# Performance work log

Measured on AMD Instinct MI355X. Metric: run time of the kernel, lower is better.

## Reference

```python
import jax, jax.numpy as jnp
import numpy as np

B, S, IN, E, L = 8, 1024, 768, 256, 12

def setup_inputs() -> dict:
    key = jax.random.key(0)
    k1, k2, k3, k4 = jax.random.split(key, 4)
    input_tensor = jax.random.normal(k1, (B, S, IN), dtype=jnp.float32)
    fc_w = jax.random.normal(k2, (E, IN), dtype=jnp.float32) * (1.0 / np.sqrt(IN))
    fc_b = jax.random.normal(k3, (E,), dtype=jnp.float32) * 0.02
    bi_w = jax.random.normal(k4, (E * L, E), dtype=jnp.float32) * (1.0 / np.sqrt(E))
    bias = jnp.zeros((E,), dtype=jnp.float32)
    return {"input_tensor": input_tensor, "fc_w": fc_w, "fc_b": fc_b, "bi_w": bi_w, "bias": bias}

def reference(input_tensor, fc_w, fc_b, bi_w, bias):
    # fc: [B,S,IN] -> [B,S,E]
    t = jnp.einsum('bsi,ei->bse', input_tensor, fc_w) + fc_b
    # bi_linear: [B,S,E] -> [B,S,L,E], plus bias over E
    bl = jnp.einsum('bse,fe->bsf', t, bi_w).reshape(B, S, L, E) + bias
    # bilinear score: out[b,i,l,j] = sum_e bl[b,i,l,e] * t[b,j,e]
    # (avoids materializing the O(B*S*S*E) expanded value tensor)
    return jnp.einsum('bile,bje->bilj', bl, t)
```

## Files before the change

kernel.cpp:

```cpp
#include <hip/hip_runtime.h>
#include <hip/hip_bf16.h>

typedef __bf16 bf16_t;
typedef __bf16 bf16x8 __attribute__((ext_vector_type(8)));
typedef __bf16 bf16x4 __attribute__((ext_vector_type(4)));
typedef float f32x4 __attribute__((ext_vector_type(4)));

#define AS1 __attribute__((address_space(1)))
#define AS3 __attribute__((address_space(3)))

__global__ __launch_bounds__(256)
void cvt_all(const float* __restrict__ in, bf16_t* __restrict__ o_in,
             const float* __restrict__ fw, bf16_t* __restrict__ o_fw,
             const float* __restrict__ bw, bf16_t* __restrict__ o_bw) {
    int i = blockIdx.x * 256 + threadIdx.x;
    const float* s;
    bf16_t* d;
    int k;
    if (i < 786432)      { s = in; d = o_in; k = i; }
    else if (i < 811008) { s = fw; d = o_fw; k = i - 786432; }
    else if (i < 909312) { s = bw; d = o_bw; k = i - 811008; }
    else return;
    float4 a = ((const float4*)s)[k * 2];
    float4 b = ((const float4*)s)[k * 2 + 1];
    bf16x8 v;
    v[0] = (bf16_t)a.x; v[1] = (bf16_t)a.y; v[2] = (bf16_t)a.z; v[3] = (bf16_t)a.w;
    v[4] = (bf16_t)b.x; v[5] = (bf16_t)b.y; v[6] = (bf16_t)b.z; v[7] = (bf16_t)b.w;
    ((bf16x8*)d)[k] = v;
}

template <int BM, int BN, int EPI>
__global__ __launch_bounds__(256)
void gemm_bt(const bf16_t* __restrict__ A, const bf16_t* __restrict__ Bm,
             void* __restrict__ Cv, const float* __restrict__ bias,
             int M, int N, int K) {
    constexpr int MR = BM / 32;
    constexpr int NR = BN / 32;
    typedef float fvec __attribute__((ext_vector_type(NR)));
    typedef bf16_t bvec __attribute__((ext_vector_type(NR)));

    __shared__ bf16_t As[BM * 64];
    __shared__ bf16_t Bs[BN * 64];

    const int tid  = threadIdx.x;
    const int lane = tid & 63;
    const int wave = tid >> 6;
    const int mblk = blockIdx.x, nblk = blockIdx.y;

    const bf16_t* Ab = A + (long)mblk * BM * K;
    const bf16_t* Bb = Bm + (long)nblk * BN * K;

    f32x4 acc[MR][NR] = {};

    const int wrow = (wave >> 1) * (BM / 2);
    const int wcol = (wave & 1) * (BN / 2);
    const int lrow = lane & 15;
    const int kgrp = lane >> 4;

    for (int k0 = 0; k0 < K; k0 += 64) {
#pragma unroll
        for (int it = 0; it < MR; ++it) {
            const int chunk = it * 256 + tid;
            const int row = chunk >> 3, c8 = chunk & 7;
            __builtin_amdgcn_global_load_lds(
                (const AS1 void*)(Ab + (long)row * K + k0 + c8 * 8),
                (AS3 void*)(As + chunk * 8), 16, 0, 0);
        }
#pragma unroll
        for (int it = 0; it < NR; ++it) {
            const int chunk = it * 256 + tid;
            const int row = chunk >> 3, c8 = chunk & 7;
            __builtin_amdgcn_global_load_lds(
                (const AS1 void*)(Bb + (long)row * K + k0 + c8 * 8),
                (AS3 void*)(Bs + chunk * 8), 16, 0, 0);
        }
        __syncthreads();

#pragma unroll
        for (int kk = 0; kk < 64; kk += 32) {
            const int koff = kk + kgrp * 8;
            bf16x8 af[MR], bfr[NR];
#pragma unroll
            for (int m = 0; m < MR; ++m)
                af[m] = *(const bf16x8*)(As + (wrow + m * 16 + lrow) * 64 + koff);
#pragma unroll
            for (int n = 0; n < NR; ++n)
                bfr[n] = *(const bf16x8*)(Bs + (wcol + lrow * NR + n) * 64 + koff);
#pragma unroll
            for (int m = 0; m < MR; ++m)
#pragma unroll
                for (int n = 0; n < NR; ++n)
                    acc[m][n] = __builtin_amdgcn_mfma_f32_16x16x32_bf16(af[m], bfr[n], acc[m][n], 0, 0, 0);
        }
        __syncthreads();
    }

    const long rbase = (long)mblk * BM + wrow + kgrp * 4;
    const long cb0   = (long)nblk * BN + wcol + lrow * NR;
    bf16_t* C = (bf16_t*)Cv;
    const float* bp = bias + cb0;
    fvec bv = *(const fvec*)bp;
#pragma unroll
    for (int m = 0; m < MR; ++m)
#pragma unroll
        for (int j = 0; j < 4; ++j) {
            bvec v;
#pragma unroll
            for (int n = 0; n < NR; ++n) v[n] = (bf16_t)(acc[m][n][j] + bv[n]);
            *(bvec*)(C + (rbase + m * 16 + j) * N + cb0) = v;
        }
}

template <int EPI, int XCD, int NMB, int NNB>
__global__ __launch_bounds__(512, 2)
void gemm8p(const bf16_t* __restrict__ A, const bf16_t* __restrict__ Bm,
            void* __restrict__ Cv, const float* __restrict__ bias,
            int N, long sA, long sB, long sC) {
    constexpr int K = 256;
    extern __shared__ bf16_t lds[];

    const int tid  = threadIdx.x;
    const int lane = tid & 63;
    const int wave = tid >> 6;
    const int wm = wave >> 2, wn = wave & 3;
    const int lrow = lane & 15, kgrp = lane >> 4;

    int mblk, nblk, bz;
    {
        int L = blockIdx.x;
        if (XCD) { bz = L & 7; int w = L >> 3; nblk = w % NNB; mblk = w / NNB; }
        else     { bz = 0;     mblk = L % NMB; nblk = L / NMB; }
    }

    const bf16_t* Ab = A + (long)bz * sA + (long)mblk * 256 * K;
    const bf16_t* Bb = Bm + (long)bz * sB + (long)nblk * 256 * K;

    const int c0 = tid, c1 = 512 + tid;
    const int r0 = c0 >> 3, r1 = c1 >> 3;
    const int ca0 = (c0 & 7) ^ (r0 & 7),        ca1 = (c1 & 7) ^ (r1 & 7);
    const int cb0 = (c0 & 7) ^ ((r0 >> 2) & 7), cb1 = (c1 & 7) ^ ((r1 >> 2) & 7);

    auto stageA = [&](int t, int h) {
        const bf16_t* s0 = Ab + (long)(h * 128 + r0) * K + t * 64 + ca0 * 8;
        const bf16_t* s1 = Ab + (long)(h * 128 + r1) * K + t * 64 + ca1 * 8;
        bf16_t* d = lds + ((t & 1) * 2 + h) * 8192;
        __builtin_amdgcn_global_load_lds((const AS1 void*)s0, (AS3 void*)(d + c0 * 8), 16, 0, 0);
        __builtin_amdgcn_global_load_lds((const AS1 void*)s1, (AS3 void*)(d + c1 * 8), 16, 0, 0);
    };
    auto stageB = [&](int t, int h) {
        const bf16_t* s0 = Bb + (long)(h * 128 + r0) * K + t * 64 + cb0 * 8;
        const bf16_t* s1 = Bb + (long)(h * 128 + r1) * K + t * 64 + cb1 * 8;
        bf16_t* d = lds + 32768 + ((t & 1) * 2 + h) * 8192;
        __builtin_amdgcn_global_load_lds((const AS1 void*)s0, (AS3 void*)(d + c0 * 8), 16, 0, 0);
        __builtin_amdgcn_global_load_lds((const AS1 void*)s1, (AS3 void*)(d + c1 * 8), 16, 0, 0);
    };
    auto ldA = [&](int t, int mf, int kk) -> bf16x8 {
        const int row = mf * 16 + lrow;
        const int col = (kk * 32 + kgrp * 8) ^ ((row & 7) << 3);
        return *(const bf16x8*)(lds + ((t & 1) * 2 + wm) * 8192 + row * 64 + col);
    };
    auto ldB = [&](int t, int g, int kk) -> bf16x8 {
        const int row = (wn & 1) * 64 + lrow * 4 + g;
        const int col = (kk * 32 + kgrp * 8) ^ (((row >> 2) & 7) << 3);
        return *(const bf16x8*)(lds + 32768 + ((t & 1) * 2 + (wn >> 1)) * 8192 + row * 64 + col);
    };

    f32x4 acc[8][4] = {};
    bf16x8 bfr[4][2];

    stageA(0, 0); stageA(0, 1); stageB(0, 0); stageB(0, 1); stageB(1, 0); stageB(1, 1);
    asm volatile("s_waitcnt vmcnt(4)" ::: "memory");
    __builtin_amdgcn_s_barrier();

#pragma unroll
    for (int i = 0; i < 2; ++i) {
#pragma unroll
        for (int p = 0; p < 8; ++p) {
            const int q = p & 3;
            const int t = 2 * i + (p >> 2);
            bf16x8 af[2][2];
            if (q == 0) {
#pragma unroll
                for (int g = 0; g < 4; ++g) { bfr[g][0] = ldB(t, g, 0); bfr[g][1] = ldB(t, g, 1); }
            }
#pragma unroll
            for (int mm = 0; mm < 2; ++mm) { af[mm][0] = ldA(t, 2 * q + mm, 0); af[mm][1] = ldA(t, 2 * q + mm, 1); }

            if (p == 0) stageA(2 * i + 1, 0);
            else if (p == 1) stageA(2 * i + 1, 1);
            else if (p == 2) { if (2 * i + 2 < 4) stageB(2 * i + 2, 0); }
            else if (p == 3) { if (2 * i + 2 < 4) stageB(2 * i + 2, 1); }
            else if (p == 4) { if (2 * i + 2 < 4) stageA(2 * i + 2, 0); }
            else if (p == 5) { if (2 * i + 2 < 4) stageA(2 * i + 2, 1); }
            else if (p == 6) { if (2 * i + 3 < 4) stageB(2 * i + 3, 0); }
            else             { if (2 * i + 3 < 4) stageB(2 * i + 3, 1); }

            __builtin_amdgcn_s_barrier();
            asm volatile("s_waitcnt lgkmcnt(0)" ::: "memory");
            __builtin_amdgcn_s_setprio(1);
#pragma unroll
            for (int mm = 0; mm < 2; ++mm)
#pragma unroll
                for (int g = 0; g < 4; ++g)
#pragma unroll
                    for (int kk = 0; kk < 2; ++kk)
                        acc[2 * q + mm][g] = __builtin_amdgcn_mfma_f32_16x16x32_bf16(
                            af[mm][kk], bfr[g][kk], acc[2 * q + mm][g], 0, 0, 0);
            __builtin_amdgcn_s_setprio(0);

            if (p == 3) {
                if (2 * i + 2 < 4) asm volatile("s_waitcnt vmcnt(4)" ::: "memory");
                else               asm volatile("s_waitcnt vmcnt(0)" ::: "memory");
            } else if (p == 7) {
                if (2 * i + 2 < 4) asm volatile("s_waitcnt vmcnt(4)" ::: "memory");
            }
            __builtin_amdgcn_s_barrier();
        }
    }

    const long rb = (long)mblk * 256 + wm * 128 + kgrp * 4;
    const long cb = (long)nblk * 256 + wn * 64 + lrow * 4;
    if constexpr (EPI == 0) {
        float* C = (float*)Cv + (long)bz * sC;
#pragma unroll
        for (int m = 0; m < 8; ++m)
#pragma unroll
            for (int j = 0; j < 4; ++j) {
                f32x4 v = { acc[m][0][j], acc[m][1][j], acc[m][2][j], acc[m][3][j] };
                __builtin_nontemporal_store(v, (f32x4*)(C + (rb + m * 16 + j) * N + cb));
            }
    } else {
        bf16_t* C = (bf16_t*)Cv;
        f32x4 bv = *(const f32x4*)(bias + (int)(cb & 255));
#pragma unroll
        for (int m = 0; m < 8; ++m)
#pragma unroll
            for (int j = 0; j < 4; ++j) {
                bf16x4 v;
#pragma unroll
                for (int g = 0; g < 4; ++g) v[g] = (bf16_t)(acc[m][g][j] + bv[g]);
                *(bf16x4*)(C + (rb + m * 16 + j) * N + cb) = v;
            }
    }
}

__global__ __launch_bounds__(256, 2)
void gemm3p(const bf16_t* __restrict__ A, const bf16_t* __restrict__ Bm,
            float* __restrict__ C, long sA, long sB, long sC) {
    extern __shared__ bf16_t lds[];
    bf16_t* Alds = lds;
    bf16_t* Blds = lds + 24576;

    const int tid  = threadIdx.x;
    const int lane = tid & 63;
    const int wave = tid >> 6;
    const int wm = wave >> 1, wn = wave & 1;
    const int lrow = lane & 15, kgrp = lane >> 4;

    const int L = blockIdx.x;
    const int bz = L & 7;
    const int mblk = L >> 3;

    const bf16_t* Ab = A + (long)bz * sA + (long)mblk * 96 * 256;
    const bf16_t* Bb = Bm + (long)bz * sB;

    auto stageB = [&](int s) {
        const int nb2 = s >> 2, t2 = s & 3, buf = s & 1;
        const bf16_t* base = Bb + (long)nb2 * 128 * 256;
#pragma unroll
        for (int it = 0; it < 4; ++it) {
            const int c = it * 256 + tid, row = c >> 3;
            const int sb = (c & 7) ^ ((row >> 2) & 7);
            __builtin_amdgcn_global_load_lds(
                (const AS1 void*)(base + (long)row * 256 + t2 * 64 + sb * 8),
                (AS3 void*)(Blds + buf * 8192 + c * 8), 16, 0, 0);
        }
    };

#pragma unroll
    for (int it = 0; it < 12; ++it) {
        const int c = it * 256 + tid;
        const int row = c >> 5, c8 = c & 31;
        const int s8 = c8 ^ (row & 7);
        __builtin_amdgcn_global_load_lds(
            (const AS1 void*)(Ab + (long)row * 256 + s8 * 8),
            (AS3 void*)(Alds + c * 8), 16, 0, 0);
    }
    stageB(0);
    asm volatile("s_waitcnt vmcnt(0)" ::: "memory");
    __builtin_amdgcn_s_barrier();

    f32x4 acc[3][4] = {};
    float* Cb = C + (long)bz * sC;
    const long rb = (long)mblk * 96 + wm * 48 + kgrp * 4;

    for (int nb = 0; nb < 8; ++nb) {
#pragma unroll
        for (int t = 0; t < 4; ++t) {
            const int s = nb * 4 + t;
            if (s < 31) stageB(s + 1);

            bf16x8 af[3][2], bfr[4][2];
#pragma unroll
            for (int m = 0; m < 3; ++m) {
                const int r = wm * 48 + m * 16 + lrow;
#pragma unroll
                for (int kk = 0; kk < 2; ++kk) {
                    const int g8 = t * 8 + kk * 4 + kgrp;
                    af[m][kk] = *(const bf16x8*)(Alds + r * 256 + (g8 ^ (r & 7)) * 8);
                }
            }
#pragma unroll
            for (int g = 0; g < 4; ++g) {
                const int r = wn * 64 + lrow * 4 + g;
#pragma unroll
                for (int kk = 0; kk < 2; ++kk)
                    bfr[g][kk] = *(const bf16x8*)(Blds + (t & 1) * 8192 + r * 64 +
                                                  ((kk * 32 + kgrp * 8) ^ (((r >> 2) & 7) << 3)));
            }

            __builtin_amdgcn_s_setprio(1);
#pragma unroll
            for (int m = 0; m < 3; ++m)
#pragma unroll
                for (int g = 0; g < 4; ++g)
#pragma unroll
                    for (int kk = 0; kk < 2; ++kk)
                        acc[m][g] = __builtin_amdgcn_mfma_f32_16x16x32_bf16(
                            af[m][kk], bfr[g][kk], acc[m][g], 0, 0, 0);
            __builtin_amdgcn_s_setprio(0);

            if (t == 3) {
                const long cb = (long)nb * 128 + wn * 64 + lrow * 4;
#pragma unroll
                for (int m = 0; m < 3; ++m)
#pragma unroll
                    for (int j = 0; j < 4; ++j) {
                        f32x4 v = { acc[m][0][j], acc[m][1][j], acc[m][2][j], acc[m][3][j] };
                        __builtin_nontemporal_store(v, (f32x4*)(Cb + (rb + m * 16 + j) * 1024 + cb));
                    }
#pragma unroll
                for (int m = 0; m < 3; ++m)
#pragma unroll
                    for (int g = 0; g < 4; ++g)
                        acc[m][g] = f32x4{0.f, 0.f, 0.f, 0.f};
            }
            __syncthreads();
        }
    }
}

extern "C" void kernel_launch(void* const* d_in, const int* in_sizes, int n_in,
                              void* d_out, int out_size, void* d_ws, size_t ws_size,
                              hipStream_t stream) {
    const float* input = (const float*)d_in[0];
    const float* fc_w  = (const float*)d_in[1];
    const float* fc_b  = (const float*)d_in[2];
    const float* bi_w  = (const float*)d_in[3];
    const float* bias  = (const float*)d_in[4];

    char* ws = (char*)d_ws;
    bf16_t* inA = (bf16_t*)(ws);
    bf16_t* wfc = (bf16_t*)(ws + 12582912);
    bf16_t* wbi = (bf16_t*)(ws + 12976128);
    bf16_t* t   = (bf16_t*)(ws + 14548992);
    bf16_t* bl  = (bf16_t*)(ws + 18743296);

    cvt_all<<<dim3(3552), dim3(256), 0, stream>>>(input, inA, fc_w, wfc, bi_w, wbi);

    gemm_bt<128, 64, 1><<<dim3(64, 4), dim3(256), 0, stream>>>(
        inA, wfc, (void*)t, fc_b, 8192, 256, 768);

    gemm8p<2, 0, 32, 12><<<dim3(384), dim3(512), 131072, stream>>>(
        t, wbi, (void*)bl, bias, 3072, 0L, 0L, 0L);

    gemm3p<<<dim3(1024), dim3(256), 81920, stream>>>(
        bl, t, (float*)d_out,
        (long)12288 * 256, (long)1024 * 256, (long)12288 * 1024);
}
```

Baseline: 131.2 us.

## Double-buffer accumulators to spread output stores across next tile's k-steps

The final bilinear GEMM now keeps two accumulator sets and alternates between them per output column block. The fp32 stores of the previous tile are spread across the four k-steps of the next tile, so they overlap with MFMA work instead of bursting at tile end. The end-of-step __syncthreads is replaced by a top-of-step partial vmcnt wait plus barrier, which lets outstanding stores stay in flight. This doubles accumulator register use, which risks spills or lower occupancy.

New measurement: 143.2 us. 9.1% more time.

```diff
diff --git a/kernel.cpp b/kernel.cpp
--- a/kernel.cpp
+++ b/kernel.cpp
@@ -245,7 +245,7 @@
 }
 
 __global__ __launch_bounds__(256, 2)
-void gemm3p(const bf16_t* __restrict__ A, const bf16_t* __restrict__ Bm,
+void gemm3q(const bf16_t* __restrict__ A, const bf16_t* __restrict__ Bm,
             float* __restrict__ C, long sA, long sB, long sC) {
     extern __shared__ bf16_t lds[];
     bf16_t* Alds = lds;
@@ -265,23 +265,22 @@
     const bf16_t* Bb = Bm + (long)bz * sB;
 
     auto stageB = [&](int s) {
-        const int nb2 = s >> 2, t2 = s & 3, buf = s & 1;
-        const bf16_t* base = Bb + (long)nb2 * 128 * 256;
+        const bf16_t* base = Bb + (long)(s >> 2) * 128 * 256;
 #pragma unroll
         for (int it = 0; it < 4; ++it) {
             const int c = it * 256 + tid, row = c >> 3;
             const int sb = (c & 7) ^ ((row >> 2) & 7);
             __builtin_amdgcn_global_load_lds(
-                (const AS1 void*)(base + (long)row * 256 + t2 * 64 + sb * 8),
-                (AS3 void*)(Blds + buf * 8192 + c * 8), 16, 0, 0);
+                (const AS1 void*)(base + (long)row * 256 + (s & 3) * 64 + sb * 8),
+                (AS3 void*)(Blds + (s & 1) * 8192 + c * 8), 16, 0, 0);
         }
     };
 
 #pragma unroll
     for (int it = 0; it < 12; ++it) {
         const int c = it * 256 + tid;
-        const int row = c >> 5, c8 = c & 31;
-        const int s8 = c8 ^ (row & 7);
+        const int row = c >> 5;
+        const int s8 = (c & 31) ^ (row & 7);
         __builtin_amdgcn_global_load_lds(
             (const AS1 void*)(Ab + (long)row * 256 + s8 * 8),
             (AS3 void*)(Alds + c * 8), 16, 0, 0);
@@ -290,16 +289,19 @@
     asm volatile("s_waitcnt vmcnt(0)" ::: "memory");
     __builtin_amdgcn_s_barrier();
 
-    f32x4 acc[3][4] = {};
+    f32x4 aE[3][4] = {}, aO[3][4] = {};
     float* Cb = C + (long)bz * sC;
     const long rb = (long)mblk * 96 + wm * 48 + kgrp * 4;
-
-    for (int nb = 0; nb < 8; ++nb) {
+    const int cbl = wn * 64 + lrow * 4;
+
+    auto tile = [&](int nb, f32x4 (&cur)[3][4], f32x4 (&prv)[3][4]) {
 #pragma unroll
         for (int t = 0; t < 4; ++t) {
             const int s = nb * 4 + t;
+            if (s <= 4) asm volatile("s_waitcnt vmcnt(0)" ::: "memory");
+            else        asm volatile("s_waitcnt vmcnt(3)" ::: "memory");
+            __builtin_amdgcn_s_barrier();
             if (s < 31) stageB(s + 1);
-
             bf16x8 af[3][2], bfr[4][2];
 #pragma unroll
             for (int m = 0; m < 3; ++m) {
@@ -315,10 +317,10 @@
                 const int r = wn * 64 + lrow * 4 + g;
 #pragma unroll
                 for (int kk = 0; kk < 2; ++kk)
-                    bfr[g][kk] = *(const bf16x8*)(Blds + (t & 1) * 8192 + r * 64 +
+                    bfr[g][kk] = *(const bf16x8*)(Blds + (s & 1) * 8192 + r * 64 +
                                                   ((kk * 32 + kgrp * 8) ^ (((r >> 2) & 7) << 3)));
             }
-
+            asm volatile("s_waitcnt lgkmcnt(0)" ::: "memory");
             __builtin_amdgcn_s_setprio(1);
 #pragma unroll
             for (int m = 0; m < 3; ++m)
@@ -326,27 +328,43 @@
                 for (int g = 0; g < 4; ++g)
 #pragma unroll
                     for (int kk = 0; kk < 2; ++kk)
-                        acc[m][g] = __builtin_amdgcn_mfma_f32_16x16x32_bf16(
-                            af[m][kk], bfr[g][kk], acc[m][g], 0, 0, 0);
+                        cur[m][g] = __builtin_amdgcn_mfma_f32_16x16x32_bf16(
+                            af[m][kk], bfr[g][kk], cur[m][g], 0, 0, 0);
             __builtin_amdgcn_s_setprio(0);
-
-            if (t == 3) {
-                const long cb = (long)nb * 128 + wn * 64 + lrow * 4;
-#pragma unroll
-                for (int m = 0; m < 3; ++m)
-#pragma unroll
-                    for (int j = 0; j < 4; ++j) {
-                        f32x4 v = { acc[m][0][j], acc[m][1][j], acc[m][2][j], acc[m][3][j] };
-                        __builtin_nontemporal_store(v, (f32x4*)(Cb + (rb + m * 16 + j) * 1024 + cb));
-                    }
-#pragma unroll
-                for (int m = 0; m < 3; ++m)
-#pragma unroll
-                    for (int g = 0; g < 4; ++g)
-                        acc[m][g] = f32x4{0.f, 0.f, 0.f, 0.f};
-            }
-            __syncthreads();
-        }
+            if (nb >= 1) {
+                const long cbP = (long)(nb - 1) * 128 + cbl;
+#pragma unroll
+                for (int k = 0; k < 3; ++k) {
+                    const int idx = t * 3 + k, m = idx >> 2, j = idx & 3;
+                    f32x4 v = { prv[m][0][j], prv[m][1][j], prv[m][2][j], prv[m][3][j] };
+                    __builtin_nontemporal_store(v, (f32x4*)(Cb + (rb + m * 16 + j) * 1024 + cbP));
+                }
+                if (t == 3) {
+#pragma unroll
+                    for (int m = 0; m < 3; ++m)
+#pragma unroll
+                        for (int g = 0; g < 4; ++g)
+                            prv[m][g] = f32x4{0.f, 0.f, 0.f, 0.f};
+                }
+            }
+        }
+    };
+
+#pragma unroll
+    for (int nb = 0; nb < 8; ++nb) {
+        if ((nb & 1) == 0) tile(nb, aE, aO);
+        else               tile(nb, aO, aE);
+    }
+
+    {
+        const long cbP = 7L * 128 + cbl;
+#pragma unroll
+        for (int m = 0; m < 3; ++m)
+#pragma unroll
+            for (int j = 0; j < 4; ++j) {
+                f32x4 v = { aO[m][0][j], aO[m][1][j], aO[m][2][j], aO[m][3][j] };
+                __builtin_nontemporal_store(v, (f32x4*)(Cb + (rb + m * 16 + j) * 1024 + cbP));
+            }
     }
 }
 
@@ -374,7 +392,7 @@
     gemm8p<2, 0, 32, 12><<<dim3(384), dim3(512), 131072, stream>>>(
         t, wbi, (void*)bl, bias, 3072, 0L, 0L, 0L);
 
-    gemm3p<<<dim3(1024), dim3(256), 81920, stream>>>(
+    gemm3q<<<dim3(1024), dim3(256), 81920, stream>>>(
         bl, t, (float*)d_out,
         (long)12288 * 256, (long)1024 * 256, (long)12288 * 1024);
 }
```
